# Optimization experiments

Hardware: AMD Instinct MI355X
Metric: run time of the kernel (lower is better)

Reference implementation:

```python
import jax, jax.numpy as jnp
import numpy as np

B, T, H, D = 4, 4096, 16, 64
BLOCK_SIZE = 64      # BS: local block size
NUM_GLOBAL = 64      # G: global tokens (first G positions)
NUM_RANDOM = 192     # R: random key positions shared by all blocks


def setup_inputs() -> dict:
    key = jax.random.key(0)
    kq, kk, kv, kr = jax.random.split(key, 4)
    q = jax.random.normal(kq, (B, T, H, D), dtype=jnp.float32)
    k = jax.random.normal(kk, (B, T, H, D), dtype=jnp.float32)
    v = jax.random.normal(kv, (B, T, H, D), dtype=jnp.float32)
    # torch.randperm(src_len)[:R] -> no duplicate indices
    rand_idx = jax.random.permutation(kr, T)[:NUM_RANDOM].astype(jnp.int32)
    return {"q": q, "k": k, "v": v, "rand_idx": rand_idx}


def _bigbird(q, k, v, rand_idx):
    Bq, Tq, Hq, Dq = q.shape
    inv_scale = Dq ** (-0.5)
    G, BS, R = NUM_GLOBAL, BLOCK_SIZE, NUM_RANDOM

    # --- global queries: full attention over all keys ---
    gs = jnp.einsum('bghd,bkhd->bhgk', q[:, :G], k) * inv_scale
    gw = jax.nn.softmax(gs, axis=-1)
    out_g = jnp.einsum('bhgk,bkhd->bghd', gw, v)  # (B, G, H, D)

    # --- non-global queries: local block + global + random keys, one softmax ---
    nb = (Tq - G) // BS  # (T - G) divisible by BS by construction
    qb = q[:, G:].reshape(Bq, nb, BS, Hq, Dq)
    kb = k[:, G:].reshape(Bq, nb, BS, Hq, Dq)
    vb = v[:, G:].reshape(Bq, nb, BS, Hq, Dq)
    kg, vg = k[:, :G], v[:, :G]            # (B, G, H, D)
    kr, vr = k[:, rand_idx], v[:, rand_idx]  # (B, R, H, D)

    s_loc = jnp.einsum('bnlhd,bnkhd->bnhlk', qb, kb)   # (B, nb, H, BS, BS)
    s_glo = jnp.einsum('bnlhd,bkhd->bnhlk', qb, kg)    # (B, nb, H, BS, G)
    s_rnd = jnp.einsum('bnlhd,bkhd->bnhlk', qb, kr)    # (B, nb, H, BS, R)
    s = jnp.concatenate([s_loc, s_glo, s_rnd], axis=-1) * inv_scale
    w = jax.nn.softmax(s, axis=-1)  # joint softmax over local|global|random keys
    w_loc, w_glo, w_rnd = w[..., :BS], w[..., BS:BS + G], w[..., BS + G:]

    out_b = (jnp.einsum('bnhlk,bnkhd->bnlhd', w_loc, vb)
             + jnp.einsum('bnhlk,bkhd->bnlhd', w_glo, vg)
             + jnp.einsum('bnhlk,bkhd->bnlhd', w_rnd, vr))
    out_b = out_b.reshape(Bq, Tq - G, Hq, Dq)

    return jnp.concatenate([out_g, out_b], axis=1)  # (B, T, H, D)


def reference(q, k, v, rand_idx):
    return _bigbird(q, k, v, rand_idx)
```

## Files before the change

### kernel.cpp

```cpp
#include <hip/hip_runtime.h>
#include <math.h>
#include <stdint.h>

#define BB 4
#define TT 4096
#define HH 16
#define DD 64
#define GG 64
#define NRND 192
#define HD 1024
#define NBH 64
#define NCHUNK 4
#define NGBLK (NBH*NCHUNK)
#define NSPB  (NBH*63)

#define OFF_KBF  0ull
#define OFF_VT   33554432ull
#define OFF_KRT  67108864ull
#define OFF_VRT  68681728ull
#define OFF_WACC 70254592ull
#define OFF_WM   74448896ull
#define OFF_WL   74514432ull

typedef __attribute__((ext_vector_type(8))) short short8;
typedef __attribute__((ext_vector_type(16))) float f32x16;

__device__ __forceinline__ ushort rne_u(float f) {
    uint32_t u = __builtin_bit_cast(uint32_t, f);
    u += 0x7fffu + ((u >> 16) & 1u);
    return (ushort)(u >> 16);
}
__device__ __forceinline__ float exp2_fast(float x) {
    float r; asm("v_exp_f32 %0, %1" : "=v"(r) : "v"(x)); return r;
}
__device__ __forceinline__ short8 ld8u(const ushort* p) {
    typedef __attribute__((ext_vector_type(4))) short short4v;
    short4v a = *(const short4v*)p;
    short4v b = *(const short4v*)(p + 4);
    short8 r;
    r[0]=a[0]; r[1]=a[1]; r[2]=a[2]; r[3]=a[3];
    r[4]=b[0]; r[5]=b[1]; r[6]=b[2]; r[7]=b[3];
    return r;
}

typedef const __attribute__((address_space(1))) uint32_t* gas1_t;
typedef __attribute__((address_space(3))) uint32_t* las3_t;
__device__ __forceinline__ void gld16(const void* g, void* l) {
    __builtin_amdgcn_global_load_lds((gas1_t)g, (las3_t)l, 16, 0, 0);
}

__global__ __launch_bounds__(256, 4)
void bb_prep(const float* __restrict__ K, const float* __restrict__ V,
             const int* __restrict__ RIDX, char* __restrict__ ws)
{
    __shared__ ushort tl[64][68];
    __shared__ int toks[NRND];
    const int bid = blockIdx.x, tid = threadIdx.x;
    const int r  = tid >> 2;
    const int d0 = (tid & 3) * 16;

    if (bid < 8192) {
        const bool isK = bid < 4096;
        const int id = isK ? bid : bid - 4096;
        const int bh = id >> 6, tile = id & 63;
        const int b = bh >> 4, h = bh & 15;
        const float* src = (isK ? K : V) + ((size_t)b*TT*HH + h)*DD
                         + (size_t)(tile*64 + r)*HD + d0;
        float f[16];
        #pragma unroll
        for (int i = 0; i < 16; i += 4) {
            const float4 v4 = *(const float4*)(src + i);
            f[i]=v4.x; f[i+1]=v4.y; f[i+2]=v4.z; f[i+3]=v4.w;
        }
        if (isK) {
            #pragma unroll
            for (int i = 0; i < 16; ++i) tl[r][d0+i] = rne_u(f[i]);
        } else {
            #pragma unroll
            for (int i = 0; i < 16; ++i) tl[d0+i][r] = rne_u(f[i]);
        }
        __syncthreads();
        char* obase = ws + (isK ? OFF_KBF : OFF_VT)
                    + (size_t)bh*524288 + (size_t)tile*8192;
        #pragma unroll
        for (int e = 0; e < 2; ++e) {
            const int uu = tid*2 + e;
            const int c = uu >> 6, rr = uu & 63;
            *(short8*)(obase + c*1024 + rr*16) = ld8u(&tl[rr][c*8]);
        }
    } else {
        const int bh = bid - 8192;
        const int b = bh >> 4, h = bh & 15;
        const size_t base = ((size_t)b*TT*HH + h)*DD;
        if (tid < NRND) toks[tid] = RIDX[tid];
        __syncthreads();
        for (int sub = 0; sub < 3; ++sub) {
            const int tok = toks[sub*64 + r];
            float f[16];
            const float* ks = K + base + (size_t)tok*HD + d0;
            #pragma unroll
            for (int i = 0; i < 16; i += 4) {
                const float4 v4 = *(const float4*)(ks + i);
                f[i]=v4.x; f[i+1]=v4.y; f[i+2]=v4.z; f[i+3]=v4.w;
            }
            #pragma unroll
            for (int i = 0; i < 16; ++i) tl[r][d0+i] = rne_u(f[i]);
            __syncthreads();
            {
                char* obase = ws + OFF_KRT + (size_t)bh*24576 + (size_t)sub*8192;
                #pragma unroll
                for (int e = 0; e < 2; ++e) {
                    const int uu = tid*2 + e;
                    const int c = uu >> 6, rr = uu & 63;
                    *(short8*)(obase + c*1024 + rr*16) = ld8u(&tl[rr][c*8]);
                }
            }
            __syncthreads();
            const float* vs = V + base + (size_t)tok*HD + d0;
            #pragma unroll
            for (int i = 0; i < 16; i += 4) {
                const float4 v4 = *(const float4*)(vs + i);
                f[i]=v4.x; f[i+1]=v4.y; f[i+2]=v4.z; f[i+3]=v4.w;
            }
            #pragma unroll
            for (int i = 0; i < 16; ++i) tl[d0+i][r] = rne_u(f[i]);
            __syncthreads();
            {
                char* obase = ws + OFF_VRT + (size_t)bh*24576 + (size_t)sub*8192;
                #pragma unroll
                for (int e = 0; e < 2; ++e) {
                    const int uu = tid*2 + e;
                    const int c = uu >> 6, rr = uu & 63;
                    *(short8*)(obase + c*1024 + rr*16) = ld8u(&tl[rr][c*8]);
                }
            }
            __syncthreads();
        }
    }
}

__global__ __launch_bounds__(256, 4)
void bb_mfma(const float* __restrict__ Q, float* __restrict__ OUT,
             char* __restrict__ ws)
{
    __shared__ __align__(16) char smem[32768];
    float (*osum)[67] = (float(*)[67])smem;
    float* sm_m0 = (float*)(smem + 17408);
    float* sm_m1 = (float*)(smem + 17664);
    float* sm_l0 = (float*)(smem + 17920);
    float* sm_l1 = (float*)(smem + 18176);

    const int tid  = threadIdx.x;
    const int lane = tid & 63;
    const int wid  = tid >> 6;
    const int wq   = wid >> 1;
    const int wk   = wid & 1;
    const int lq   = lane & 31;
    const int lh   = lane >> 5;

    const int j  = blockIdx.x;
    const int x  = j & 7;
    const int t  = j >> 3;
    const int bh_local = t / 67;
    const int sub      = t - bh_local * 67;
    const int bh = x * 8 + bh_local;
    const bool is_glob = sub < NCHUNK;
    int qtok0, ntiles, kt0 = 0, chunk = 0;
    if (is_glob) {
        chunk = sub;
        kt0   = chunk * 16;
        qtok0 = 0; ntiles = 16;
    } else {
        qtok0 = GG + (sub - NCHUNK) * 64;
        ntiles = 5;
    }
    const int b  = bh >> 4;
    const int hd = bh & 15;
    const size_t bh_off = ((size_t)b * TT * HH + hd) * DD;

    const char* kbf_bh = ws + OFF_KBF + (size_t)bh * 524288;
    const char* vt_bh  = ws + OFF_VT  + (size_t)bh * 524288;
    const char* krt_bh = ws + OFF_KRT + (size_t)bh * 24576;
    const char* vrt_bh = ws + OFF_VRT + (size_t)bh * 24576;

    auto kbase = [&](int kt) -> const char* {
        if (is_glob)     return kbf_bh + (size_t)(kt0 + kt) * 8192;
        if (kt == 0)     return kbf_bh + (size_t)(qtok0 >> 6) * 8192;
        if (kt == 1)     return kbf_bh;
        return krt_bh + (size_t)(kt - 2) * 8192;
    };
    auto vbase = [&](int kt) -> const char* {
        if (is_glob)     return vt_bh + (size_t)(kt0 + kt) * 8192;
        if (kt == 0)     return vt_bh + (size_t)(qtok0 >> 6) * 8192;
        if (kt == 1)     return vt_bh;
        return vrt_bh + (size_t)(kt - 2) * 8192;
    };

    float4 qa[4], qb[4];
    {
        const float* qp = Q + bh_off + (size_t)(qtok0 + wq*32 + lq) * HD;
        #pragma unroll
        for (int ks = 0; ks < 4; ++ks) {
            qa[ks] = *(const float4*)(qp + ks*16 + lh*8);
            qb[ks] = *(const float4*)(qp + ks*16 + lh*8 + 4);
        }
    }

    auto stage = [&](int buf, int kt_t) {
        const char* kb = kbase(kt_t);
        const char* vb = vbase(kt_t);
        #pragma unroll
        for (int i = 0; i < 2; ++i) {
            const int c = wid*2 + i;
            gld16(kb + c*1024 + lane*16, smem + buf*8192 + c*1024);
            gld16(vb + c*1024 + lane*16, smem + 16384 + buf*8192 + c*1024);
        }
    };
    stage(0, 0);

    const float QSC = 0.18033688f;
    short8 qf[4];
    #pragma unroll
    for (int ks = 0; ks < 4; ++ks) {
        float fv[8] = {qa[ks].x, qa[ks].y, qa[ks].z, qa[ks].w,
                       qb[ks].x, qb[ks].y, qb[ks].z, qb[ks].w};
        #pragma unroll
        for (int jj = 0; jj < 8; ++jj)
            qf[ks][jj] = (short)rne_u(fv[jj] * QSC);
    }

    f32x16 acc0, acc1;
    #pragma unroll
    for (int r = 0; r < 16; ++r) { acc0[r] = 0.f; acc1[r] = 0.f; }
    float m_run = -INFINITY, l_run = 0.f;

    for (int kt = 0; kt < ntiles; ++kt) {
        const int cur = kt & 1;
        const bool hn = (kt + 1 < ntiles);
        if (hn) {
            stage(cur ^ 1, kt + 1);
            asm volatile("s_waitcnt vmcnt(4)" ::: "memory");
        } else {
            asm volatile("s_waitcnt vmcnt(0)" ::: "memory");
        }
        __builtin_amdgcn_s_barrier();
        asm volatile("" ::: "memory");

        const char* kb = smem + cur*8192;
        const char* vb = smem + 16384 + cur*8192;

        f32x16 sc;
        #pragma unroll
        for (int r = 0; r < 16; ++r) sc[r] = 0.f;
        {
            const int krow = wk*32 + lq;
            __builtin_amdgcn_s_setprio(1);
            #pragma unroll
            for (int ks = 0; ks < 4; ++ks) {
                const short8 ak = *(const short8*)(kb + (ks*2 + lh)*1024 + krow*16);
                sc = __builtin_amdgcn_mfma_f32_32x32x16_bf16(ak, qf[ks], sc, 0, 0, 0);
            }
            __builtin_amdgcn_s_setprio(0);
        }

        float pm = sc[0];
        #pragma unroll
        for (int r = 1; r < 16; ++r) pm = fmaxf(pm, sc[r]);
        pm = fmaxf(pm, __shfl_xor(pm, 32));
        if (__any(pm > m_run + 11.5f)) {
            const float mnew = fmaxf(m_run, pm);
            const float cf = exp2_fast(m_run - mnew);
            l_run *= cf;
            #pragma unroll
            for (int r = 0; r < 16; ++r) { acc0[r] *= cf; acc1[r] *= cf; }
            m_run = mnew;
        }
        float ls = 0.f;
        #pragma unroll
        for (int r = 0; r < 16; ++r) {
            sc[r] = exp2_fast(sc[r] - m_run);
            ls += sc[r];
        }
        ls += __shfl_xor(ls, 32);
        l_run += ls;

        #pragma unroll
        for (int s = 0; s < 2; ++s) {
            uint32_t a01, a23, a45, a67;
            asm("v_cvt_pk_bf16_f32 %0, %1, %2" : "=v"(a01) : "v"(sc[8*s+0]), "v"(sc[8*s+1]));
            asm("v_cvt_pk_bf16_f32 %0, %1, %2" : "=v"(a23) : "v"(sc[8*s+2]), "v"(sc[8*s+3]));
            asm("v_cvt_pk_bf16_f32 %0, %1, %2" : "=v"(a45) : "v"(sc[8*s+4]), "v"(sc[8*s+5]));
            asm("v_cvt_pk_bf16_f32 %0, %1, %2" : "=v"(a67) : "v"(sc[8*s+6]), "v"(sc[8*s+7]));
            asm("v_permlane32_swap_b32 %0, %1" : "+v"(a01), "+v"(a45));
            asm("v_permlane32_swap_b32 %0, %1" : "+v"(a23), "+v"(a67));
            union { uint32_t u[4]; short8 v; } pfu;
            pfu.u[0] = a01; pfu.u[1] = a23; pfu.u[2] = a45; pfu.u[3] = a67;
            const int cb = wk*4 + s*2 + lh;
            const short8 v0 = *(const short8*)(vb + cb*1024 + lq*16);
            const short8 v1 = *(const short8*)(vb + cb*1024 + (lq + 32)*16);
            __builtin_amdgcn_s_setprio(1);
            acc0 = __builtin_amdgcn_mfma_f32_32x32x16_bf16(v0, pfu.v, acc0, 0, 0, 0);
            acc1 = __builtin_amdgcn_mfma_f32_32x32x16_bf16(v1, pfu.v, acc1, 0, 0, 0);
            __builtin_amdgcn_s_setprio(0);
        }

        if (hn) {
            asm volatile("" ::: "memory");
            __builtin_amdgcn_s_barrier();
            asm volatile("" ::: "memory");
        }
    }

    __syncthreads();
    const int qrow = wq*32 + lq;
    if (lane < 32) {
        (wk ? sm_m1 : sm_m0)[qrow] = m_run;
        (wk ? sm_l1 : sm_l0)[qrow] = l_run;
    }
    __syncthreads();
    const float Mq  = fmaxf(sm_m0[qrow], sm_m1[qrow]);
    const float wsc = exp2_fast(m_run - Mq);
    if (wk == 0) {
        #pragma unroll
        for (int r = 0; r < 16; ++r) {
            const int dr = (r & 3) + 8*(r >> 2) + 4*lh;
            osum[qrow][dr     ] = acc0[r] * wsc;
            osum[qrow][dr + 32] = acc1[r] * wsc;
        }
    }
    __syncthreads();
    if (wk == 1) {
        #pragma unroll
        for (int r = 0; r < 16; ++r) {
            const int dr = (r & 3) + 8*(r >> 2) + 4*lh;
            osum[qrow][dr     ] += acc0[r] * wsc;
            osum[qrow][dr + 32] += acc1[r] * wsc;
        }
    }
    __syncthreads();
    {
        const int q  = tid >> 2;
        const int d0 = (tid & 3) * 16;
        const float M     = fmaxf(sm_m0[q], sm_m1[q]);
        const float lcomb = exp2_fast(sm_m0[q] - M) * sm_l0[q]
                          + exp2_fast(sm_m1[q] - M) * sm_l1[q];
        if (is_glob) {
            float* WACC = (float*)(ws + OFF_WACC);
            float* WM   = (float*)(ws + OFF_WM);
            float* WL   = (float*)(ws + OFF_WL);
            const int slot = chunk * NBH + bh;
            float* dst = WACC + (size_t)slot * 4096 + q * 64 + d0;
            #pragma unroll
            for (int i = 0; i < 16; i += 4) {
                float4 o;
                o.x = osum[q][d0 + i    ];
                o.y = osum[q][d0 + i + 1];
                o.z = osum[q][d0 + i + 2];
                o.w = osum[q][d0 + i + 3];
                *(float4*)(dst + i) = o;
            }
            if ((tid & 3) == 0) {
                WM[slot * 64 + q] = M;
                WL[slot * 64 + q] = lcomb;
            }
        } else {
            const float inv = 1.f / lcomb;
            float* dst = OUT + bh_off + (size_t)(qtok0 + q) * HD + d0;
            #pragma unroll
            for (int i = 0; i < 16; i += 4) {
                float4 o;
                o.x = osum[q][d0 + i    ] * inv;
                o.y = osum[q][d0 + i + 1] * inv;
                o.z = osum[q][d0 + i + 2] * inv;
                o.w = osum[q][d0 + i + 3] * inv;
                *(float4*)(dst + i) = o;
            }
        }
    }
}

__global__ __launch_bounds__(64, 8)
void bb_combine(const char* __restrict__ ws, float* __restrict__ OUT)
{
    const int bid = blockIdx.x;
    const int bh  = bid >> 2;
    const int qq  = bid & 3;
    const int b   = bh >> 4;
    const int hd  = bh & 15;
    const size_t bh_off = ((size_t)b * TT * HH + hd) * DD;

    const float* WACC = (const float*)(ws + OFF_WACC);
    const float* WM   = (const float*)(ws + OFF_WM);
    const float* WL   = (const float*)(ws + OFF_WL);

    const int tid = threadIdx.x;
    const int q  = qq * 16 + (tid >> 2);
    const int d0 = (tid & 3) * 16;

    float m[NCHUNK];
    float M = -INFINITY;
    #pragma unroll
    for (int c = 0; c < NCHUNK; ++c) {
        m[c] = WM[(c * NBH + bh) * 64 + q];
        M = fmaxf(M, m[c]);
    }
    float w[NCHUNK];
    float denom = 0.f;
    #pragma unroll
    for (int c = 0; c < NCHUNK; ++c) {
        w[c] = exp2_fast(m[c] - M);
        denom += w[c] * WL[(c * NBH + bh) * 64 + q];
    }
    const float inv = 1.f / denom;

    float* dst = OUT + bh_off + (size_t)q * HD + d0;
    #pragma unroll
    for (int i = 0; i < 16; i += 4) {
        float ox = 0.f, oy = 0.f, oz = 0.f, ow = 0.f;
        #pragma unroll
        for (int c = 0; c < NCHUNK; ++c) {
            const float4 a = *(const float4*)&WACC[(size_t)(c * NBH + bh) * 4096 + q * 64 + d0 + i];
            ox += w[c] * a.x; oy += w[c] * a.y;
            oz += w[c] * a.z; ow += w[c] * a.w;
        }
        float4 o; o.x = ox * inv; o.y = oy * inv; o.z = oz * inv; o.w = ow * inv;
        *(float4*)(dst + i) = o;
    }
}

extern "C" void kernel_launch(void* const* d_in, const int* in_sizes, int n_in,
                              void* d_out, int out_size, void* d_ws, size_t ws_size,
                              hipStream_t stream) {
    const float* Q    = (const float*)d_in[0];
    const float* K    = (const float*)d_in[1];
    const float* V    = (const float*)d_in[2];
    const int*   RIDX = (const int*)d_in[3];
    float* OUT = (float*)d_out;
    char*  ws  = (char*)d_ws;

    hipLaunchKernelGGL(bb_prep, dim3(8192 + 64), dim3(256), 0, stream,
                       K, V, RIDX, ws);
    hipLaunchKernelGGL(bb_mfma, dim3(NGBLK + NSPB), dim3(256), 0, stream,
                       Q, OUT, ws);
    hipLaunchKernelGGL(bb_combine, dim3(NBH * 4), dim3(64), 0, stream, ws, OUT);
}
```

Before: 111.8 us.

## Pair adjacent query blocks per workgroup to share global and random key tiles

Each sparse workgroup now handles two consecutive 64-query blocks, loading the shared global and random K/V tiles once and applying them to both query sets. Each block's local tile is handled separately. This cuts the redundant staging of the shared tiles roughly in half and reduces the grid size. In exchange, every thread holds a second set of accumulators and Q fragments, so launch bounds drop to 2 waves per SIMD, lowering occupancy. The pair path also adds a second epilogue with extra barriers.

New measurement: 136.9 us. 1.22x slower.

```diff
diff --git a/kernel.cpp b/kernel.cpp
--- a/kernel.cpp
+++ b/kernel.cpp
@@ -11,8 +11,7 @@
 #define HD 1024
 #define NBH 64
 #define NCHUNK 4
-#define NGBLK (NBH*NCHUNK)
-#define NSPB  (NBH*63)
+#define SUBS 36
 
 #define OFF_KBF  0ull
 #define OFF_VT   33554432ull
@@ -139,7 +138,7 @@
     }
 }
 
-__global__ __launch_bounds__(256, 4)
+__global__ __launch_bounds__(256, 2)
 void bb_mfma(const float* __restrict__ Q, float* __restrict__ OUT,
              char* __restrict__ ws)
 {
@@ -157,21 +156,28 @@
     const int wk   = wid & 1;
     const int lq   = lane & 31;
     const int lh   = lane >> 5;
+    const int qrow = wq*32 + lq;
 
     const int j  = blockIdx.x;
     const int x  = j & 7;
     const int t  = j >> 3;
-    const int bh_local = t / 67;
-    const int sub      = t - bh_local * 67;
+    const int bh_local = t / SUBS;
+    const int sub      = t - bh_local * SUBS;
     const int bh = x * 8 + bh_local;
     const bool is_glob = sub < NCHUNK;
-    int qtok0, ntiles, kt0 = 0, chunk = 0;
+    const bool is_pair = (sub >= NCHUNK) && (sub < 35);
+    int qtok0A = 0, qtok0B = 0, ntiles, kt0 = 0, chunk = 0, tA = 0, tB = 0;
     if (is_glob) {
-        chunk = sub;
-        kt0   = chunk * 16;
-        qtok0 = 0; ntiles = 16;
+        chunk = sub; kt0 = chunk * 16; ntiles = 16;
+    } else if (is_pair) {
+        const int qi0 = (sub - NCHUNK) * 2;
+        qtok0A = GG + qi0 * 64;
+        qtok0B = qtok0A + 64;
+        tA = 1 + qi0; tB = 2 + qi0;
+        ntiles = 6;
     } else {
-        qtok0 = GG + (sub - NCHUNK) * 64;
+        qtok0A = GG + 62 * 64;
+        tA = 63;
         ntiles = 5;
     }
     const int b  = bh >> 4;
@@ -184,27 +190,29 @@
     const char* vrt_bh = ws + OFF_VRT + (size_t)bh * 24576;
 
     auto kbase = [&](int kt) -> const char* {
-        if (is_glob)     return kbf_bh + (size_t)(kt0 + kt) * 8192;
-        if (kt == 0)     return kbf_bh + (size_t)(qtok0 >> 6) * 8192;
-        if (kt == 1)     return kbf_bh;
+        if (is_glob) return kbf_bh + (size_t)(kt0 + kt) * 8192;
+        if (is_pair) {
+            if (kt == 0) return kbf_bh + (size_t)tA * 8192;
+            if (kt == 1) return kbf_bh + (size_t)tB * 8192;
+            if (kt == 2) return kbf_bh;
+            return krt_bh + (size_t)(kt - 3) * 8192;
+        }
+        if (kt == 0) return kbf_bh + (size_t)tA * 8192;
+        if (kt == 1) return kbf_bh;
         return krt_bh + (size_t)(kt - 2) * 8192;
     };
     auto vbase = [&](int kt) -> const char* {
-        if (is_glob)     return vt_bh + (size_t)(kt0 + kt) * 8192;
-        if (kt == 0)     return vt_bh + (size_t)(qtok0 >> 6) * 8192;
-        if (kt == 1)     return vt_bh;
+        if (is_glob) return vt_bh + (size_t)(kt0 + kt) * 8192;
+        if (is_pair) {
+            if (kt == 0) return vt_bh + (size_t)tA * 8192;
+            if (kt == 1) return vt_bh + (size_t)tB * 8192;
+            if (kt == 2) return vt_bh;
+            return vrt_bh + (size_t)(kt - 3) * 8192;
+        }
+        if (kt == 0) return vt_bh + (size_t)tA * 8192;
+        if (kt == 1) return vt_bh;
         return vrt_bh + (size_t)(kt - 2) * 8192;
     };
-
-    float4 qa[4], qb[4];
-    {
-        const float* qp = Q + bh_off + (size_t)(qtok0 + wq*32 + lq) * HD;
-        #pragma unroll
-        for (int ks = 0; ks < 4; ++ks) {
-            qa[ks] = *(const float4*)(qp + ks*16 + lh*8);
-            qb[ks] = *(const float4*)(qp + ks*16 + lh*8 + 4);
-        }
-    }
 
     auto stage = [&](int buf, int kt_t) {
         const char* kb = kbase(kt_t);
@@ -219,36 +227,39 @@
     stage(0, 0);
 
     const float QSC = 0.18033688f;
-    short8 qf[4];
+    short8 qfA[4], qfB[4];
+    {
+        const float* qp = Q + bh_off + (size_t)((is_glob ? 0 : qtok0A) + qrow) * HD;
+        #pragma unroll
+        for (int ks = 0; ks < 4; ++ks) {
+            const float4 fa = *(const float4*)(qp + ks*16 + lh*8);
+            const float4 fb = *(const float4*)(qp + ks*16 + lh*8 + 4);
+            float fv[8] = {fa.x,fa.y,fa.z,fa.w, fb.x,fb.y,fb.z,fb.w};
+            #pragma unroll
+            for (int jj = 0; jj < 8; ++jj)
+                qfA[ks][jj] = (short)rne_u(fv[jj] * QSC);
+        }
+    }
+    if (is_pair) {
+        const float* qp = Q + bh_off + (size_t)(qtok0B + qrow) * HD;
+        #pragma unroll
+        for (int ks = 0; ks < 4; ++ks) {
+            const float4 fa = *(const float4*)(qp + ks*16 + lh*8);
+            const float4 fb = *(const float4*)(qp + ks*16 + lh*8 + 4);
+            float fv[8] = {fa.x,fa.y,fa.z,fa.w, fb.x,fb.y,fb.z,fb.w};
+            #pragma unroll
+            for (int jj = 0; jj < 8; ++jj)
+                qfB[ks][jj] = (short)rne_u(fv[jj] * QSC);
+        }
+    }
+
+    f32x16 accA0, accA1, accB0, accB1;
     #pragma unroll
-    for (int ks = 0; ks < 4; ++ks) {
-        float fv[8] = {qa[ks].x, qa[ks].y, qa[ks].z, qa[ks].w,
-                       qb[ks].x, qb[ks].y, qb[ks].z, qb[ks].w};
-        #pragma unroll
-        for (int jj = 0; jj < 8; ++jj)
-            qf[ks][jj] = (short)rne_u(fv[jj] * QSC);
-    }
-
-    f32x16 acc0, acc1;
-    #pragma unroll
-    for (int r = 0; r < 16; ++r) { acc0[r] = 0.f; acc1[r] = 0.f; }
-    float m_run = -INFINITY, l_run = 0.f;
-
-    for (int kt = 0; kt < ntiles; ++kt) {
-        const int cur = kt & 1;
-        const bool hn = (kt + 1 < ntiles);
-        if (hn) {
-            stage(cur ^ 1, kt + 1);
-            asm volatile("s_waitcnt vmcnt(4)" ::: "memory");
-        } else {
-            asm volatile("s_waitcnt vmcnt(0)" ::: "memory");
-        }
-        __builtin_amdgcn_s_barrier();
-        asm volatile("" ::: "memory");
-
-        const char* kb = smem + cur*8192;
-        const char* vb = smem + 16384 + cur*8192;
-
+    for (int r = 0; r < 16; ++r) { accA0[r]=0.f; accA1[r]=0.f; accB0[r]=0.f; accB1[r]=0.f; }
+    float mA = -INFINITY, lA = 0.f, mB = -INFINITY, lB = 0.f;
+
+    auto do_qset = [&](const short8* qf, f32x16& a0, f32x16& a1,
+                       float& mr, float& lr, const char* kb, const char* vb) {
         f32x16 sc;
         #pragma unroll
         for (int r = 0; r < 16; ++r) sc[r] = 0.f;
@@ -262,28 +273,26 @@
             }
             __builtin_amdgcn_s_setprio(0);
         }
-
         float pm = sc[0];
         #pragma unroll
         for (int r = 1; r < 16; ++r) pm = fmaxf(pm, sc[r]);
         pm = fmaxf(pm, __shfl_xor(pm, 32));
-        if (__any(pm > m_run + 11.5f)) {
-            const float mnew = fmaxf(m_run, pm);
-            const float cf = exp2_fast(m_run - mnew);
-            l_run *= cf;
-            #pragma unroll
-            for (int r = 0; r < 16; ++r) { acc0[r] *= cf; acc1[r] *= cf; }
-            m_run = mnew;
+        if (__any(pm > mr + 11.5f)) {
+            const float mnew = fmaxf(mr, pm);
+            const float cf = exp2_fast(mr - mnew);
+            lr *= cf;
+            #pragma unroll
+            for (int r = 0; r < 16; ++r) { a0[r] *= cf; a1[r] *= cf; }
+            mr = mnew;
         }
         float ls = 0.f;
         #pragma unroll
         for (int r = 0; r < 16; ++r) {
-            sc[r] = exp2_fast(sc[r] - m_run);
+            sc[r] = exp2_fast(sc[r] - mr);
             ls += sc[r];
         }
         ls += __shfl_xor(ls, 32);
-        l_run += ls;
-
+        lr += ls;
         #pragma unroll
         for (int s = 0; s < 2; ++s) {
             uint32_t a01, a23, a45, a67;
@@ -299,9 +308,36 @@
             const short8 v0 = *(const short8*)(vb + cb*1024 + lq*16);
             const short8 v1 = *(const short8*)(vb + cb*1024 + (lq + 32)*16);
             __builtin_amdgcn_s_setprio(1);
-            acc0 = __builtin_amdgcn_mfma_f32_32x32x16_bf16(v0, pfu.v, acc0, 0, 0, 0);
-            acc1 = __builtin_amdgcn_mfma_f32_32x32x16_bf16(v1, pfu.v, acc1, 0, 0, 0);
+            a0 = __builtin_amdgcn_mfma_f32_32x32x16_bf16(v0, pfu.v, a0, 0, 0, 0);
+            a1 = __builtin_amdgcn_mfma_f32_32x32x16_bf16(v1, pfu.v, a1, 0, 0, 0);
             __builtin_amdgcn_s_setprio(0);
+        }
+    };
+
+    for (int kt = 0; kt < ntiles; ++kt) {
+        const int cur = kt & 1;
+        const bool hn = (kt + 1 < ntiles);
+        if (hn) {
+            stage(cur ^ 1, kt + 1);
+            asm volatile("s_waitcnt vmcnt(4)" ::: "memory");
+        } else {
+            asm volatile("s_waitcnt vmcnt(0)" ::: "memory");
+        }
+        __builtin_amdgcn_s_barrier();
+        asm volatile("" ::: "memory");
+
+        const char* kb = smem + cur*8192;
+        const char* vb = smem + 16384 + cur*8192;
+
+        if (is_pair) {
+            if (kt == 0)      do_qset(qfA, accA0, accA1, mA, lA, kb, vb);
+            else if (kt == 1) do_qset(qfB, accB0, accB1, mB, lB, kb, vb);
+            else {
+                do_qset(qfA, accA0, accA1, mA, lA, kb, vb);
+                do_qset(qfB, accB0, accB1, mB, lB, kb, vb);
+            }
+        } else {
+            do_qset(qfA, accA0, accA1, mA, lA, kb, vb);
         }
 
         if (hn) {
@@ -311,72 +347,76 @@
         }
     }
 
-    __syncthreads();
-    const int qrow = wq*32 + lq;
-    if (lane < 32) {
-        (wk ? sm_m1 : sm_m0)[qrow] = m_run;
-        (wk ? sm_l1 : sm_l0)[qrow] = l_run;
-    }
-    __syncthreads();
-    const float Mq  = fmaxf(sm_m0[qrow], sm_m1[qrow]);
-    const float wsc = exp2_fast(m_run - Mq);
-    if (wk == 0) {
-        #pragma unroll
-        for (int r = 0; r < 16; ++r) {
-            const int dr = (r & 3) + 8*(r >> 2) + 4*lh;
-            osum[qrow][dr     ] = acc0[r] * wsc;
-            osum[qrow][dr + 32] = acc1[r] * wsc;
-        }
-    }
-    __syncthreads();
-    if (wk == 1) {
-        #pragma unroll
-        for (int r = 0; r < 16; ++r) {
-            const int dr = (r & 3) + 8*(r >> 2) + 4*lh;
-            osum[qrow][dr     ] += acc0[r] * wsc;
-            osum[qrow][dr + 32] += acc1[r] * wsc;
-        }
-    }
-    __syncthreads();
-    {
-        const int q  = tid >> 2;
-        const int d0 = (tid & 3) * 16;
-        const float M     = fmaxf(sm_m0[q], sm_m1[q]);
-        const float lcomb = exp2_fast(sm_m0[q] - M) * sm_l0[q]
-                          + exp2_fast(sm_m1[q] - M) * sm_l1[q];
-        if (is_glob) {
-            float* WACC = (float*)(ws + OFF_WACC);
-            float* WM   = (float*)(ws + OFF_WM);
-            float* WL   = (float*)(ws + OFF_WL);
-            const int slot = chunk * NBH + bh;
-            float* dst = WACC + (size_t)slot * 4096 + q * 64 + d0;
-            #pragma unroll
-            for (int i = 0; i < 16; i += 4) {
-                float4 o;
-                o.x = osum[q][d0 + i    ];
-                o.y = osum[q][d0 + i + 1];
-                o.z = osum[q][d0 + i + 2];
-                o.w = osum[q][d0 + i + 3];
-                *(float4*)(dst + i) = o;
-            }
-            if ((tid & 3) == 0) {
-                WM[slot * 64 + q] = M;
-                WL[slot * 64 + q] = lcomb;
-            }
-        } else {
-            const float inv = 1.f / lcomb;
-            float* dst = OUT + bh_off + (size_t)(qtok0 + q) * HD + d0;
-            #pragma unroll
-            for (int i = 0; i < 16; i += 4) {
-                float4 o;
-                o.x = osum[q][d0 + i    ] * inv;
-                o.y = osum[q][d0 + i + 1] * inv;
-                o.z = osum[q][d0 + i + 2] * inv;
-                o.w = osum[q][d0 + i + 3] * inv;
-                *(float4*)(dst + i) = o;
-            }
-        }
-    }
+    auto epilogue = [&](f32x16& a0, f32x16& a1, float mr, float lr, int qtok0x) {
+        __syncthreads();
+        if (lane < 32) {
+            (wk ? sm_m1 : sm_m0)[qrow] = mr;
+            (wk ? sm_l1 : sm_l0)[qrow] = lr;
+        }
+        __syncthreads();
+        const float Mq  = fmaxf(sm_m0[qrow], sm_m1[qrow]);
+        const float wsc = exp2_fast(mr - Mq);
+        if (wk == 0) {
+            #pragma unroll
+            for (int r = 0; r < 16; ++r) {
+                const int dr = (r & 3) + 8*(r >> 2) + 4*lh;
+                osum[qrow][dr     ] = a0[r] * wsc;
+                osum[qrow][dr + 32] = a1[r] * wsc;
+            }
+        }
+        __syncthreads();
+        if (wk == 1) {
+            #pragma unroll
+            for (int r = 0; r < 16; ++r) {
+                const int dr = (r & 3) + 8*(r >> 2) + 4*lh;
+                osum[qrow][dr     ] += a0[r] * wsc;
+                osum[qrow][dr + 32] += a1[r] * wsc;
+            }
+        }
+        __syncthreads();
+        {
+            const int q  = tid >> 2;
+            const int d0 = (tid & 3) * 16;
+            const float M     = fmaxf(sm_m0[q], sm_m1[q]);
+            const float lcomb = exp2_fast(sm_m0[q] - M) * sm_l0[q]
+                              + exp2_fast(sm_m1[q] - M) * sm_l1[q];
+            if (is_glob) {
+                float* WACC = (float*)(ws + OFF_WACC);
+                float* WM   = (float*)(ws + OFF_WM);
+                float* WL   = (float*)(ws + OFF_WL);
+                const int slot = chunk * NBH + bh;
+                float* dst = WACC + (size_t)slot * 4096 + q * 64 + d0;
+                #pragma unroll
+                for (int i = 0; i < 16; i += 4) {
+                    float4 o;
+                    o.x = osum[q][d0 + i    ];
+                    o.y = osum[q][d0 + i + 1];
+                    o.z = osum[q][d0 + i + 2];
+                    o.w = osum[q][d0 + i + 3];
+                    *(float4*)(dst + i) = o;
+                }
+                if ((tid & 3) == 0) {
+                    WM[slot * 64 + q] = M;
+                    WL[slot * 64 + q] = lcomb;
+                }
+            } else {
+                const float inv = 1.f / lcomb;
+                float* dst = OUT + bh_off + (size_t)(qtok0x + q) * HD + d0;
+                #pragma unroll
+                for (int i = 0; i < 16; i += 4) {
+                    float4 o;
+                    o.x = osum[q][d0 + i    ] * inv;
+                    o.y = osum[q][d0 + i + 1] * inv;
+                    o.z = osum[q][d0 + i + 2] * inv;
+                    o.w = osum[q][d0 + i + 3] * inv;
+                    *(float4*)(dst + i) = o;
+                }
+            }
+        }
+    };
+
+    epilogue(accA0, accA1, mA, lA, qtok0A);
+    if (is_pair) epilogue(accB0, accB1, mB, lB, qtok0B);
 }
 
 __global__ __launch_bounds__(64, 8)
@@ -440,7 +480,7 @@
 
     hipLaunchKernelGGL(bb_prep, dim3(8192 + 64), dim3(256), 0, stream,
                        K, V, RIDX, ws);
-    hipLaunchKernelGGL(bb_mfma, dim3(NGBLK + NSPB), dim3(256), 0, stream,
+    hipLaunchKernelGGL(bb_mfma, dim3(NBH * SUBS), dim3(256), 0, stream,
                        Q, OUT, ws);
     hipLaunchKernelGGL(bb_combine, dim3(NBH * 4), dim3(64), 0, stream, ws, OUT);
 }
```
